# Optimization experiments

Measured on AMD Instinct MI355X. Metric: run time of the kernel, lower is better.

Reference implementation:

```python
import jax, jax.numpy as jnp
import numpy as np

B = 512      # graphs per batch
NPG = 62     # nodes (electrodes) per graph
N = B * NPG  # total nodes per band
F_IN = 5     # node features
H = 8        # attention heads
C = 3        # num_classes (GATConv out channels, concat=False)
DEG = 16     # avg degree
EG = NPG * DEG
E = B * EG   # edges per band
NB = 5       # bands: delta, alpha, beta, theta, gamma
DE_DIM = 930 # 310*3


def setup_inputs() -> dict:
    key = jax.random.key(0)
    ks = jax.random.split(key, 24)
    x_bands = jax.random.normal(ks[0], (NB, N, F_IN), dtype=jnp.float32)
    # within-graph random edges: node ids in [g*62, g*62+62)
    base = (jnp.arange(B, dtype=jnp.int32) * NPG)[None, :, None]
    src = jax.random.randint(ks[1], (NB, B, EG), 0, NPG, dtype=jnp.int32) + base
    dst = jax.random.randint(ks[2], (NB, B, EG), 0, NPG, dtype=jnp.int32) + base
    edge_index_bands = jnp.stack([src.reshape(NB, E), dst.reshape(NB, E)], axis=1)  # [NB,2,E]
    batch = jnp.repeat(jnp.arange(B, dtype=jnp.int32), NPG)  # [N]
    de = jax.random.normal(ks[3], (B, NPG, 5, 3), dtype=jnp.float32)
    s = 0.3
    params = dict(
        bn_gamma=jnp.ones((NB, F_IN), jnp.float32),
        bn_beta=jnp.zeros((NB, F_IN), jnp.float32),
        W=jax.random.normal(ks[4], (NB, F_IN, H * C)) * s,
        att_src=jax.random.normal(ks[5], (NB, H, C)) * s,
        att_dst=jax.random.normal(ks[6], (NB, H, C)) * s,
        gat_bias=jax.random.normal(ks[7], (NB, C)) * 0.01,
        fg_W=jax.random.normal(ks[8], (NB * C, 64)) * s,
        fg_b=jnp.zeros((64,), jnp.float32),
        ln_g=jnp.ones((DE_DIM,), jnp.float32),
        ln_b=jnp.zeros((DE_DIM,), jnp.float32),
        q_W=jax.random.normal(ks[9], (DE_DIM, 64)) * 0.03,
        q_b=jnp.zeros((64,), jnp.float32),
        k_W=jax.random.normal(ks[10], (DE_DIM, 64)) * 0.03,
        k_b=jnp.zeros((64,), jnp.float32),
        v_W=jax.random.normal(ks[11], (DE_DIM, 64)) * 0.03,
        v_b=jnp.zeros((64,), jnp.float32),
        fa_W=jax.random.normal(ks[12], (128, C)) * s,
        fa_b=jnp.zeros((C,), jnp.float32),
    )
    return dict(x_bands=x_bands, edge_index_bands=edge_index_bands, batch=batch, de=de, **params)


def _gat_band(x, ei, g, b, Wb, a_src, a_dst, bias, batch):
    # BatchNorm1d (training-mode batch stats), eps=1e-5
    mu = x.mean(0)
    var = x.var(0)
    xn = (x - mu) * jax.lax.rsqrt(var + 1e-5) * g + b
    # GATConv(F_IN -> C, heads=H, concat=False) with self-loops
    xt = (xn @ Wb).reshape(N, H, C)                       # [N,H,C]
    al_s = (xt * a_src).sum(-1)                           # [N,H]
    al_d = (xt * a_dst).sum(-1)                           # [N,H]
    loop = jnp.arange(N, dtype=ei.dtype)
    src = jnp.concatenate([ei[0], loop])                  # [E+N]
    dst = jnp.concatenate([ei[1], loop])
    e = jax.nn.leaky_relu(al_s[src] + al_d[dst], 0.2)     # [E+N,H]
    m = jax.ops.segment_max(e, dst, num_segments=N)
    ex = jnp.exp(e - m[dst])
    denom = jax.ops.segment_sum(ex, dst, num_segments=N)  # [N,H]
    msg = ex[:, :, None] * xt[src]                        # [E+N,H,C]
    out = jax.ops.segment_sum(msg, dst, num_segments=N) / denom[:, :, None]
    out = out.mean(1) + bias                              # concat=False -> head mean
    out = jax.nn.elu(out)
    # global_mean_pool
    summed = jax.ops.segment_sum(out, batch, num_segments=B)
    cnt = jax.ops.segment_sum(jnp.ones((N,), out.dtype), batch, num_segments=B)
    return summed / cnt[:, None]                          # [B,C]


def reference(x_bands, edge_index_bands, batch, de, bn_gamma, bn_beta, W,
              att_src, att_dst, gat_bias, fg_W, fg_b, ln_g, ln_b,
              q_W, q_b, k_W, k_b, v_W, v_b, fa_W, fa_b):
    pooled = jax.vmap(_gat_band, in_axes=(0, 0, 0, 0, 0, 0, 0, 0, None))(
        x_bands, edge_index_bands, bn_gamma, bn_beta, W, att_src, att_dst, gat_bias, batch
    )  # [NB,B,C]
    x_concat = jnp.transpose(pooled, (1, 0, 2)).reshape(B, NB * C)  # [B,15]
    x_out = jax.nn.elu(x_concat @ fg_W + fg_b)                       # [B,64]
    # de branch: LayerNorm + self-attention
    de_f = de.reshape(B, DE_DIM)
    mu = de_f.mean(-1, keepdims=True)
    var = de_f.var(-1, keepdims=True)
    de_n = (de_f - mu) * jax.lax.rsqrt(var + 1e-5) * ln_g + ln_b
    Q = de_n @ q_W + q_b
    K = de_n @ k_W + k_b
    V = de_n @ v_W + v_b
    attn = jax.nn.softmax(Q @ K.T / jnp.sqrt(jnp.float32(64)), axis=-1)
    x_de = attn @ V                                                  # [B,64]
    # F.leaky_relu(x, negative_slope=1) is the identity
    out = jnp.concatenate([x_out, x_de], axis=1) @ fa_W + fa_b       # [B,3]
    return jax.nn.elu(out)
```

## Files before the change

### kernel.cpp

```cpp
#include <hip/hip_runtime.h>
#include <math.h>

#define NBANDS 5
#define BATCH  512
#define NPG    62
#define NTOT   (BATCH*NPG)
#define F_IN   5
#define NH     8
#define NC     3
#define HC     (NH*NC)
#define EG     (NPG*16)
#define ETOT   (BATCH*EG)
#define EPG    (EG+NPG)
#define DE_DIM 930
#define KS     5
#define KLEN   186

#define GAT_BLOCKS  (BATCH*NBANDS)
#define QKVP_BLOCKS (128*3*KS)
#define MID_BLOCKS  (GAT_BLOCKS + QKVP_BLOCKS)

#define WS_BN     0
#define WS_LNS    512
#define WS_POOLED 1536
#define WS_Q      (WS_POOLED + NBANDS*BATCH*NC)
#define WS_KT     (WS_Q  + BATCH*64)
#define WS_V      (WS_KT + BATCH*64)
#define WS_PART   (WS_V  + BATCH*64)
#define WS_END    (WS_PART + 3*KS*BATCH*64)

__device__ __forceinline__ float eluf(float x) { return x > 0.f ? x : expm1f(x); }

__global__ __launch_bounds__(256) void stats_kernel(
    const float* __restrict__ x, const float* __restrict__ de,
    float* __restrict__ ws) {
    int bid = blockIdx.x;
    int tid = threadIdx.x;
    int w = tid >> 6, lane = tid & 63;
    if (bid < 40) {
        int band = bid >> 3, chunk = bid & 7;
        const int G4 = NTOT / 8 / 4;
        const float4* xb4 =
            (const float4*)(x + (size_t)band * NTOT * F_IN) + (size_t)chunk * G4 * 5;
        float s[F_IN] = {0,0,0,0,0}, q[F_IN] = {0,0,0,0,0};
        for (int gi = tid; gi < G4; gi += 256) {
            const float4* p4 = xb4 + (size_t)gi * 5;
            float vv[20];
            *(float4*)&vv[0]  = p4[0];
            *(float4*)&vv[4]  = p4[1];
            *(float4*)&vv[8]  = p4[2];
            *(float4*)&vv[12] = p4[3];
            *(float4*)&vv[16] = p4[4];
            #pragma unroll
            for (int i = 0; i < 20; ++i) { float v = vv[i]; s[i % 5] += v; q[i % 5] += v * v; }
        }
        #pragma unroll
        for (int f = 0; f < F_IN; ++f) {
            for (int off = 32; off; off >>= 1) {
                s[f] += __shfl_down(s[f], off, 64);
                q[f] += __shfl_down(q[f], off, 64);
            }
        }
        __shared__ float part[4][10];
        if (lane == 0) {
            #pragma unroll
            for (int f = 0; f < F_IN; ++f) { part[w][f] = s[f]; part[w][5 + f] = q[f]; }
        }
        __syncthreads();
        if (tid < 10) {
            float t = part[0][tid] + part[1][tid] + part[2][tid] + part[3][tid];
            ws[WS_BN + (band * 8 + chunk) * 10 + tid] = t;
        }
    } else {
        int r = (bid - 40) * 4 + w;
        const float* row = de + (size_t)r * DE_DIM;
        float s1 = 0.f, s2 = 0.f;
        for (int i = lane; i < DE_DIM; i += 64) { float v = row[i]; s1 += v; s2 += v * v; }
        #pragma unroll
        for (int off = 32; off; off >>= 1) {
            s1 += __shfl_down(s1, off, 64);
            s2 += __shfl_down(s2, off, 64);
        }
        if (lane == 0) {
            float mu  = s1 * (1.0f / DE_DIM);
            float var = s2 * (1.0f / DE_DIM) - mu * mu;
            ws[WS_LNS + r * 2]     = mu;
            ws[WS_LNS + r * 2 + 1] = rsqrtf(var + 1e-5f);
        }
    }
}

struct GatShared {
    float  Wl[F_IN * HC];
    float  attS[HC], attD[HC];
    float  bnsum[10];
    float  scale[F_IN], shift[F_IN];
    float  xns[NPG * F_IN];
    float4 xt4[NPG * NH];
    float  ald[NPG * NH];
    int    deg[NPG];
    int    offs[NPG + 1];
    int    cur[NPG];
    int    csr[EPG];
    float  outd[NPG][NC];
};
struct QkvShared { float dl[4][KLEN]; };

__global__ __launch_bounds__(256) void mid_kernel(
    const float* __restrict__ x, const int* __restrict__ ei,
    const float* __restrict__ bn_g, const float* __restrict__ bn_b,
    const float* __restrict__ Wg, const float* __restrict__ attSg,
    const float* __restrict__ attDg, const float* __restrict__ biasg,
    const float* __restrict__ de, const float* __restrict__ ln_g,
    const float* __restrict__ ln_b,
    const float* __restrict__ qW, const float* __restrict__ kW,
    const float* __restrict__ vW,
    const float* __restrict__ ws_in, float* __restrict__ ws_out) {
    __shared__ __align__(16) unsigned char smem[sizeof(GatShared)];
    int bid = blockIdx.x;
    int tid = threadIdx.x;

    if (bid < GAT_BLOCKS) {
        GatShared& S = *reinterpret_cast<GatShared*>(smem);
        int g    = bid & 511;
        int band = bid >> 9;
        int lane = tid & 63;
        int nbase = g * NPG;
        const float* wsbn = ws_in + WS_BN;
        float* pooled = ws_out + WS_POOLED;

        if (tid < F_IN * HC) S.Wl[tid] = Wg[band * F_IN * HC + tid];
        if (tid >= 128 && tid < 128 + HC) S.attS[tid - 128] = attSg[band * HC + tid - 128];
        if (tid >= 160 && tid < 160 + HC) S.attD[tid - 160] = attDg[band * HC + tid - 160];
        if (tid < NPG) S.deg[tid] = 0;
        if (tid >= 192 && tid < 202) {
            int f = tid - 192;
            float t = 0.f;
            #pragma unroll
            for (int c = 0; c < 8; ++c) t += wsbn[(band * 8 + c) * 10 + f];
            S.bnsum[f] = t;
        }
        __syncthreads();

        const int* srcp = ei + (size_t)band * 2 * ETOT + (size_t)g * EG;
        const int* dstp = srcp + ETOT;

        for (int e = tid; e < EG; e += 256) atomicAdd(&S.deg[dstp[e] - nbase], 1);
        if (tid < F_IN) {
            float mu  = S.bnsum[tid] * (1.0f / NTOT);
            float var = S.bnsum[5 + tid] * (1.0f / NTOT) - mu * mu;
            float sc  = rsqrtf(var + 1e-5f) * bn_g[band * F_IN + tid];
            S.scale[tid] = sc;
            S.shift[tid] = bn_b[band * F_IN + tid] - mu * sc;
        }
        __syncthreads();

        {
            const float* xr = x + (size_t)band * NTOT * F_IN + (size_t)nbase * F_IN;
            for (int i = tid; i < NPG * F_IN; i += 256) {
                int f = i % F_IN;
                S.xns[i] = xr[i] * S.scale[f] + S.shift[f];
            }
        }
        if (tid >= 64 && tid < 128) {
            int l = lane;
            int dv = (l < NPG) ? S.deg[l] + 1 : 0;
            int sc = dv;
            #pragma unroll
            for (int off = 1; off < 64; off <<= 1) {
                int t = __shfl_up(sc, off, 64);
                if (l >= off) sc += t;
            }
            if (l < NPG) S.offs[l + 1] = sc;
            if (l == 0)  S.offs[0] = 0;
        }
        __syncthreads();

        for (int p = tid; p < NPG * NH; p += 256) {
            int n = p >> 3, h = p & 7;
            float c0 = 0.f, c1 = 0.f, c2 = 0.f;
            #pragma unroll
            for (int f = 0; f < F_IN; ++f) {
                float xv = S.xns[n * F_IN + f];
                c0 += xv * S.Wl[f * HC + h * NC + 0];
                c1 += xv * S.Wl[f * HC + h * NC + 1];
                c2 += xv * S.Wl[f * HC + h * NC + 2];
            }
            float as = c0 * S.attS[h * NC] + c1 * S.attS[h * NC + 1] + c2 * S.attS[h * NC + 2];
            float ad = c0 * S.attD[h * NC] + c1 * S.attD[h * NC + 1] + c2 * S.attD[h * NC + 2];
            S.xt4[p] = make_float4(c0, c1, c2, as);
            S.ald[p] = ad;
        }
        if (tid < NPG) { int o0 = S.offs[tid]; S.csr[o0] = tid; S.cur[tid] = o0 + 1; }
        __syncthreads();

        for (int e = tid; e < EG; e += 256) {
            int ld = dstp[e] - nbase;
            int p = atomicAdd(&S.cur[ld], 1);
            S.csr[p] = srcp[e] - nbase;
        }
        __syncthreads();

        for (int p = tid; p < NPG * NH; p += 256) {
            int d = p >> 3, h = p & 7;
            int s0 = S.offs[d], s1 = S.offs[d + 1];
            float adv = S.ald[p];
            float den = 0.f, m0 = 0.f, m1 = 0.f, m2 = 0.f;
            for (int e = s0; e < s1; ++e) {
                int s = S.csr[e];
                float4 t = S.xt4[(s << 3) + h];
                float v = t.w + adv;
                v = v > 0.f ? v : 0.2f * v;
                float ex = __expf(v);
                den += ex;
                m0 += ex * t.x;
                m1 += ex * t.y;
                m2 += ex * t.z;
            }
            float rd = 1.0f / den;
            float o0 = m0 * rd, o1 = m1 * rd, o2 = m2 * rd;
            #pragma unroll
            for (int off = 1; off < 8; off <<= 1) {
                o0 += __shfl_xor(o0, off, 64);
                o1 += __shfl_xor(o1, off, 64);
                o2 += __shfl_xor(o2, off, 64);
            }
            if (h == 0) { S.outd[d][0] = o0; S.outd[d][1] = o1; S.outd[d][2] = o2; }
        }
        __syncthreads();

        float oc[NC] = {0.f, 0.f, 0.f};
        if (tid < NPG) {
            #pragma unroll
            for (int c = 0; c < NC; ++c)
                oc[c] = eluf(S.outd[tid][c] * (1.0f / NH) + biasg[band * NC + c]);
        }
        if (tid < 64) {
            #pragma unroll
            for (int c = 0; c < NC; ++c) {
                float v = oc[c];
                for (int off = 32; off; off >>= 1) v += __shfl_down(v, off, 64);
                if (tid == 0)
                    pooled[((size_t)band * BATCH + g) * NC + c] = v * (1.0f / NPG);
            }
        }
    } else {
        QkvShared& P = *reinterpret_cast<QkvShared*>(smem);
        int q  = bid - GAT_BLOCKS;
        int ks = q / 384;
        int r3 = q - ks * 384;
        int m  = r3 >> 7;
        int rt = r3 & 127;
        const float* lns = ws_in + WS_LNS;
        float* part = ws_out + WS_PART;

        int w = tid >> 6, col = tid & 63;
        for (int i = tid; i < 4 * KLEN; i += 256) {
            int rr = i / KLEN, ii = i - rr * KLEN;
            int row = rt * 4 + rr, gcol = ks * KLEN + ii;
            float mu = lns[row * 2], rstd = lns[row * 2 + 1];
            P.dl[rr][ii] = (de[(size_t)row * DE_DIM + gcol] - mu) * rstd * ln_g[gcol] + ln_b[gcol];
        }
        __syncthreads();
        const float* Wm = ((m == 0) ? qW : (m == 1) ? kW : vW) + (size_t)ks * KLEN * 64;
        float a[6] = {0, 0, 0, 0, 0, 0};
        for (int i = 0; i < KLEN; i += 6) {
            #pragma unroll
            for (int j = 0; j < 6; ++j)
                a[j] += P.dl[w][i + j] * Wm[(size_t)(i + j) * 64 + col];
        }
        float acc = ((a[0] + a[1]) + (a[2] + a[3])) + (a[4] + a[5]);
        part[(((size_t)m * KS + ks) * BATCH + rt * 4 + w) * 64 + col] = acc;
    }
}

__global__ __launch_bounds__(256) void qkv_reduce(
    const float* __restrict__ part,
    const float* __restrict__ qb, const float* __restrict__ kb,
    const float* __restrict__ vb,
    float* __restrict__ Q, float* __restrict__ KT, float* __restrict__ V) {
    int idx = blockIdx.x * 256 + threadIdx.x;
    int m  = idx >> 15;
    int local = idx & 32767;
    if (m == 1) {
        int row = local & 511, col = local >> 9;
        float s = 0.f;
        #pragma unroll
        for (int ks = 0; ks < KS; ++ks)
            s += part[(((size_t)KS + ks) << 15) + (row << 6) + col];
        KT[local] = s + kb[col];
    } else {
        int col = local & 63;
        float s = 0.f;
        #pragma unroll
        for (int ks = 0; ks < KS; ++ks)
            s += part[(((size_t)m * KS + ks) << 15) + local];
        s += (m == 0) ? qb[col] : vb[col];
        ((m == 0) ? Q : V)[local] = s;
    }
}

__global__ __launch_bounds__(256) void qkv_fused_fb(
    const float* __restrict__ de, const float* __restrict__ ln_g,
    const float* __restrict__ ln_b,
    const float* __restrict__ qW, const float* __restrict__ qb,
    const float* __restrict__ kW, const float* __restrict__ kb,
    const float* __restrict__ vW, const float* __restrict__ vb,
    float* __restrict__ Q, float* __restrict__ KT, float* __restrict__ V) {
    int r0 = blockIdx.x * 4;
    int m  = blockIdx.y;
    __shared__ float dn[4][DE_DIM];
    int tid  = threadIdx.x;
    int w    = tid >> 6, lane = tid & 63;
    const float* row = de + (size_t)(r0 + w) * DE_DIM;
    float s1 = 0.f, s2 = 0.f;
    for (int i = lane; i < DE_DIM; i += 64) {
        float v = row[i]; dn[w][i] = v; s1 += v; s2 += v * v;
    }
    #pragma unroll
    for (int off = 32; off; off >>= 1) {
        s1 += __shfl_down(s1, off, 64);
        s2 += __shfl_down(s2, off, 64);
    }
    float mu   = __shfl(s1, 0, 64) * (1.0f / DE_DIM);
    float var  = __shfl(s2, 0, 64) * (1.0f / DE_DIM) - mu * mu;
    float rstd = rsqrtf(var + 1e-5f);
    for (int i = lane; i < DE_DIM; i += 64)
        dn[w][i] = (dn[w][i] - mu) * rstd * ln_g[i] + ln_b[i];
    __syncthreads();
    const float* Wm = (m == 0) ? qW : (m == 1) ? kW : vW;
    const float* bm = (m == 0) ? qb : (m == 1) ? kb : vb;
    float a[10];
    #pragma unroll
    for (int j = 0; j < 10; ++j) a[j] = 0.f;
    for (int i = 0; i < DE_DIM; i += 10) {
        #pragma unroll
        for (int j = 0; j < 10; ++j)
            a[j] += dn[w][i + j] * Wm[(size_t)(i + j) * 64 + lane];
    }
    float acc = (((a[0] + a[1]) + (a[2] + a[3])) + ((a[4] + a[5]) + (a[6] + a[7])))
              + (a[8] + a[9]) + bm[lane];
    int r = r0 + w;
    if (m == 1) KT[lane * BATCH + r] = acc;
    else ((m == 0) ? Q : V)[(size_t)r * 64 + lane] = acc;
}

__global__ __launch_bounds__(256) void attn_final(
    const float* __restrict__ Q, const float* __restrict__ KT,
    const float* __restrict__ V, const float* __restrict__ pooled,
    const float* __restrict__ fgW, const float* __restrict__ fgb,
    const float* __restrict__ faW, const float* __restrict__ fab,
    float* __restrict__ out) {
    int b = blockIdx.x;
    int tid = threadIdx.x;
    __shared__ float qrow[64];
    __shared__ float p[BATCH];
    __shared__ float red[8];
    __shared__ float pv[4][64];
    __shared__ float xde[64], xout[64];
    if (tid < 64) qrow[tid] = Q[(size_t)b * 64 + tid];
    __syncthreads();

    float a0 = 0.f, a1 = 0.f, b0 = 0.f, b1 = 0.f;
    #pragma unroll 8
    for (int i = 0; i < 64; i += 2) {
        float q0 = qrow[i], q1 = qrow[i + 1];
        a0 += q0 * KT[(size_t)i * BATCH + tid];
        a1 += q1 * KT[(size_t)(i + 1) * BATCH + tid];
        b0 += q0 * KT[(size_t)i * BATCH + tid + 256];
        b1 += q1 * KT[(size_t)(i + 1) * BATCH + tid + 256];
    }
    float sj0 = (a0 + a1) * 0.125f, sj1 = (b0 + b1) * 0.125f;

    float mx = fmaxf(sj0, sj1);
    for (int off = 32; off; off >>= 1) mx = fmaxf(mx, __shfl_down(mx, off, 64));
    if ((tid & 63) == 0) red[tid >> 6] = mx;
    __syncthreads();
    mx = fmaxf(fmaxf(red[0], red[1]), fmaxf(red[2], red[3]));
    float e0 = __expf(sj0 - mx), e1 = __expf(sj1 - mx);
    p[tid] = e0; p[tid + 256] = e1;
    float s = e0 + e1;
    for (int off = 32; off; off >>= 1) s += __shfl_down(s, off, 64);
    if ((tid & 63) == 0) red[4 + (tid >> 6)] = s;
    __syncthreads();
    float denom = red[4] + red[5] + red[6] + red[7];

    int o = tid & 63, cq = tid >> 6;
    float acc = 0.f;
    #pragma unroll 4
    for (int j = cq * 128; j < cq * 128 + 128; ++j)
        acc += p[j] * V[(size_t)j * 64 + o];
    pv[cq][o] = acc;
    __syncthreads();
    if (tid < 64)
        xde[tid] = (pv[0][tid] + pv[1][tid] + pv[2][tid] + pv[3][tid]) / denom;
    if (tid >= 64 && tid < 128) {
        int oo = tid - 64;
        float a = fgb[oo];
        #pragma unroll
        for (int j = 0; j < NBANDS * NC; ++j) {
            int band = j / NC, c = j % NC;
            a += pooled[((size_t)band * BATCH + b) * NC + c] * fgW[j * 64 + oo];
        }
        xout[oo] = eluf(a);
    }
    __syncthreads();
    if (tid < NC) {
        float a = fab[tid];
        for (int i = 0; i < 64; ++i) a += xout[i] * faW[i * NC + tid];
        for (int i = 0; i < 64; ++i) a += xde[i] * faW[(64 + i) * NC + tid];
        out[(size_t)b * NC + tid] = eluf(a);
    }
}

extern "C" void kernel_launch(void* const* d_in, const int* in_sizes, int n_in,
                              void* d_out, int out_size, void* d_ws, size_t ws_size,
                              hipStream_t stream) {
    const float* x     = (const float*)d_in[0];
    const int*   ei    = (const int*)  d_in[1];
    const float* de    = (const float*)d_in[3];
    const float* bn_g  = (const float*)d_in[4];
    const float* bn_b  = (const float*)d_in[5];
    const float* W     = (const float*)d_in[6];
    const float* attS  = (const float*)d_in[7];
    const float* attD  = (const float*)d_in[8];
    const float* gbias = (const float*)d_in[9];
    const float* fgW   = (const float*)d_in[10];
    const float* fgb   = (const float*)d_in[11];
    const float* ln_g  = (const float*)d_in[12];
    const float* ln_b  = (const float*)d_in[13];
    const float* qW    = (const float*)d_in[14];
    const float* qb    = (const float*)d_in[15];
    const float* kW    = (const float*)d_in[16];
    const float* kb    = (const float*)d_in[17];
    const float* vW    = (const float*)d_in[18];
    const float* vb    = (const float*)d_in[19];
    const float* faW   = (const float*)d_in[20];
    const float* fab   = (const float*)d_in[21];
    float* ws  = (float*)d_ws;
    float* out = (float*)d_out;

    stats_kernel<<<168, 256, 0, stream>>>(x, de, ws);

    if (ws_size >= (size_t)WS_END * sizeof(float)) {
        mid_kernel<<<MID_BLOCKS, 256, 0, stream>>>(
            x, ei, bn_g, bn_b, W, attS, attD, gbias,
            de, ln_g, ln_b, qW, kW, vW, ws, ws);
        qkv_reduce<<<(3 * BATCH * 64) / 256, 256, 0, stream>>>(
            ws + WS_PART, qb, kb, vb, ws + WS_Q, ws + WS_KT, ws + WS_V);
    } else {
        mid_kernel<<<GAT_BLOCKS, 256, 0, stream>>>(
            x, ei, bn_g, bn_b, W, attS, attD, gbias,
            de, ln_g, ln_b, qW, kW, vW, ws, ws);
        qkv_fused_fb<<<dim3(BATCH / 4, 3), 256, 0, stream>>>(
            de, ln_g, ln_b, qW, qb, kW, kb, vW, vb,
            ws + WS_Q, ws + WS_KT, ws + WS_V);
    }
    attn_final<<<BATCH, 256, 0, stream>>>(ws + WS_Q, ws + WS_KT, ws + WS_V,
                                          ws + WS_POOLED, fgW, fgb, faW, fab, out);
}
```

Baseline: 78.16 us.

## Pad GAT feature table in LDS, shrink CSR to ushort, split block paths into noinline functions

Pads the per-node float4 feature table in shared memory to a stride of 9 heads, so the random neighbour gathers hit fewer LDS bank conflicts. Stores the CSR neighbour list as unsigned short to cut shared-memory footprint. Moves the GAT and QKV block paths into separate noinline device functions, so each path is register-allocated on its own. Also folds the BatchNorm scale computation into the first phase and reorders the barriers. That folding reads values written by other lanes of the same wave with no barrier in between, so it relies on in-order LDS execution within a wave.

```diff
diff --git a/kernel.cpp b/kernel.cpp
--- a/kernel.cpp
+++ b/kernel.cpp
@@ -15,6 +15,7 @@
 #define DE_DIM 930
 #define KS     5
 #define KLEN   186
+#define XTS    9
 
 #define GAT_BLOCKS  (BATCH*NBANDS)
 #define QKVP_BLOCKS (128*3*KS)
@@ -91,20 +92,185 @@
 }
 
 struct GatShared {
+    float4 xt4[NPG * XTS];
     float  Wl[F_IN * HC];
     float  attS[HC], attD[HC];
     float  bnsum[10];
     float  scale[F_IN], shift[F_IN];
     float  xns[NPG * F_IN];
-    float4 xt4[NPG * NH];
     float  ald[NPG * NH];
     int    deg[NPG];
     int    offs[NPG + 1];
     int    cur[NPG];
-    int    csr[EPG];
+    unsigned short csr[EPG];
     float  outd[NPG][NC];
 };
 struct QkvShared { float dl[4][KLEN]; };
+union  MidShared { GatShared g; QkvShared q; };
+
+__device__ __noinline__ void gat_path(
+    GatShared& S, int bid,
+    const float* __restrict__ x, const int* __restrict__ ei,
+    const float* __restrict__ bn_g, const float* __restrict__ bn_b,
+    const float* __restrict__ Wg, const float* __restrict__ attSg,
+    const float* __restrict__ attDg, const float* __restrict__ biasg,
+    const float* __restrict__ wsbn, float* __restrict__ pooled) {
+    int g    = bid & 511;
+    int band = bid >> 9;
+    int tid  = threadIdx.x;
+    int lane = tid & 63;
+    int nbase = g * NPG;
+
+    if (tid < F_IN * HC) S.Wl[tid] = Wg[band * F_IN * HC + tid];
+    if (tid >= 128 && tid < 128 + HC) S.attS[tid - 128] = attSg[band * HC + tid - 128];
+    if (tid >= 160 && tid < 160 + HC) S.attD[tid - 160] = attDg[band * HC + tid - 160];
+    if (tid < NPG) S.deg[tid] = 0;
+    if (tid >= 192 && tid < 202) {
+        int f = tid - 192;
+        float t = 0.f;
+        #pragma unroll
+        for (int c = 0; c < 8; ++c) t += wsbn[(band * 8 + c) * 10 + f];
+        S.bnsum[f] = t;
+    }
+    if (tid >= 192 && tid < 192 + F_IN) {
+        int f = tid - 192;
+        float mu  = S.bnsum[f] * (1.0f / NTOT);
+        float var = S.bnsum[5 + f] * (1.0f / NTOT) - mu * mu;
+        float sc  = rsqrtf(var + 1e-5f) * bn_g[band * F_IN + f];
+        S.scale[f] = sc;
+        S.shift[f] = bn_b[band * F_IN + f] - mu * sc;
+    }
+    __syncthreads();
+
+    const int* srcp = ei + (size_t)band * 2 * ETOT + (size_t)g * EG;
+    const int* dstp = srcp + ETOT;
+
+    for (int e = tid; e < EG; e += 256) atomicAdd(&S.deg[dstp[e] - nbase], 1);
+    {
+        const float* xr = x + (size_t)band * NTOT * F_IN + (size_t)nbase * F_IN;
+        for (int i = tid; i < NPG * F_IN; i += 256) {
+            int f = i % F_IN;
+            S.xns[i] = xr[i] * S.scale[f] + S.shift[f];
+        }
+    }
+    __syncthreads();
+
+    if (tid >= 64 && tid < 128) {
+        int l = lane;
+        int dv = (l < NPG) ? S.deg[l] + 1 : 0;
+        int sc = dv;
+        #pragma unroll
+        for (int off = 1; off < 64; off <<= 1) {
+            int t = __shfl_up(sc, off, 64);
+            if (l >= off) sc += t;
+        }
+        if (l < NPG) S.offs[l + 1] = sc;
+        if (l == 0)  S.offs[0] = 0;
+    }
+    for (int p = tid; p < NPG * NH; p += 256) {
+        int n = p >> 3, h = p & 7;
+        float c0 = 0.f, c1 = 0.f, c2 = 0.f;
+        #pragma unroll
+        for (int f = 0; f < F_IN; ++f) {
+            float xv = S.xns[n * F_IN + f];
+            c0 += xv * S.Wl[f * HC + h * NC + 0];
+            c1 += xv * S.Wl[f * HC + h * NC + 1];
+            c2 += xv * S.Wl[f * HC + h * NC + 2];
+        }
+        float as = c0 * S.attS[h * NC] + c1 * S.attS[h * NC + 1] + c2 * S.attS[h * NC + 2];
+        float ad = c0 * S.attD[h * NC] + c1 * S.attD[h * NC + 1] + c2 * S.attD[h * NC + 2];
+        S.xt4[n * XTS + h] = make_float4(c0, c1, c2, as);
+        S.ald[p] = ad;
+    }
+    __syncthreads();
+
+    if (tid < NPG) {
+        int o0 = S.offs[tid];
+        S.csr[o0] = (unsigned short)tid;
+        S.cur[tid] = o0 + 1;
+    }
+    __syncthreads();
+
+    for (int e = tid; e < EG; e += 256) {
+        int ld = dstp[e] - nbase;
+        int p = atomicAdd(&S.cur[ld], 1);
+        S.csr[p] = (unsigned short)(srcp[e] - nbase);
+    }
+    __syncthreads();
+
+    for (int p = tid; p < NPG * NH; p += 256) {
+        int d = p >> 3, h = p & 7;
+        int s0 = S.offs[d], s1 = S.offs[d + 1];
+        float adv = S.ald[p];
+        float den = 0.f, m0 = 0.f, m1 = 0.f, m2 = 0.f;
+        for (int e = s0; e < s1; ++e) {
+            int s = S.csr[e];
+            float4 t = S.xt4[s * XTS + h];
+            float v = t.w + adv;
+            v = fmaxf(v, 0.2f * v);
+            float ex = __expf(v);
+            den += ex;
+            m0 += ex * t.x;
+            m1 += ex * t.y;
+            m2 += ex * t.z;
+        }
+        float rd = 1.0f / den;
+        float o0 = m0 * rd, o1 = m1 * rd, o2 = m2 * rd;
+        #pragma unroll
+        for (int off = 1; off < 8; off <<= 1) {
+            o0 += __shfl_xor(o0, off, 64);
+            o1 += __shfl_xor(o1, off, 64);
+            o2 += __shfl_xor(o2, off, 64);
+        }
+        if (h == 0) { S.outd[d][0] = o0; S.outd[d][1] = o1; S.outd[d][2] = o2; }
+    }
+    __syncthreads();
+
+    float oc[NC] = {0.f, 0.f, 0.f};
+    if (tid < NPG) {
+        #pragma unroll
+        for (int c = 0; c < NC; ++c)
+            oc[c] = eluf(S.outd[tid][c] * (1.0f / NH) + biasg[band * NC + c]);
+    }
+    if (tid < 64) {
+        #pragma unroll
+        for (int c = 0; c < NC; ++c) {
+            float v = oc[c];
+            for (int off = 32; off; off >>= 1) v += __shfl_down(v, off, 64);
+            if (tid == 0)
+                pooled[((size_t)band * BATCH + g) * NC + c] = v * (1.0f / NPG);
+        }
+    }
+}
+
+__device__ __noinline__ void qkv_path(
+    QkvShared& P, int q,
+    const float* __restrict__ de, const float* __restrict__ lns,
+    const float* __restrict__ ln_g, const float* __restrict__ ln_b,
+    const float* __restrict__ qW, const float* __restrict__ kW,
+    const float* __restrict__ vW, float* __restrict__ part) {
+    int ks = q / 384;
+    int r3 = q - ks * 384;
+    int m  = r3 >> 7;
+    int rt = r3 & 127;
+    int tid = threadIdx.x, w = tid >> 6, col = tid & 63;
+    for (int i = tid; i < 4 * KLEN; i += 256) {
+        int rr = i / KLEN, ii = i - rr * KLEN;
+        int row = rt * 4 + rr, gcol = ks * KLEN + ii;
+        float mu = lns[row * 2], rstd = lns[row * 2 + 1];
+        P.dl[rr][ii] = (de[(size_t)row * DE_DIM + gcol] - mu) * rstd * ln_g[gcol] + ln_b[gcol];
+    }
+    __syncthreads();
+    const float* Wm = ((m == 0) ? qW : (m == 1) ? kW : vW) + (size_t)ks * KLEN * 64;
+    float a[6] = {0, 0, 0, 0, 0, 0};
+    for (int i = 0; i < KLEN; i += 6) {
+        #pragma unroll
+        for (int j = 0; j < 6; ++j)
+            a[j] += P.dl[w][i + j] * Wm[(size_t)(i + j) * 64 + col];
+    }
+    float acc = ((a[0] + a[1]) + (a[2] + a[3])) + (a[4] + a[5]);
+    part[(((size_t)m * KS + ks) * BATCH + rt * 4 + w) * 64 + col] = acc;
+}
 
 __global__ __launch_bounds__(256) void mid_kernel(
     const float* __restrict__ x, const int* __restrict__ ei,
@@ -116,161 +282,14 @@
     const float* __restrict__ qW, const float* __restrict__ kW,
     const float* __restrict__ vW,
     const float* __restrict__ ws_in, float* __restrict__ ws_out) {
-    __shared__ __align__(16) unsigned char smem[sizeof(GatShared)];
+    __shared__ MidShared S;
     int bid = blockIdx.x;
-    int tid = threadIdx.x;
-
     if (bid < GAT_BLOCKS) {
-        GatShared& S = *reinterpret_cast<GatShared*>(smem);
-        int g    = bid & 511;
-        int band = bid >> 9;
-        int lane = tid & 63;
-        int nbase = g * NPG;
-        const float* wsbn = ws_in + WS_BN;
-        float* pooled = ws_out + WS_POOLED;
-
-        if (tid < F_IN * HC) S.Wl[tid] = Wg[band * F_IN * HC + tid];
-        if (tid >= 128 && tid < 128 + HC) S.attS[tid - 128] = attSg[band * HC + tid - 128];
-        if (tid >= 160 && tid < 160 + HC) S.attD[tid - 160] = attDg[band * HC + tid - 160];
-        if (tid < NPG) S.deg[tid] = 0;
-        if (tid >= 192 && tid < 202) {
-            int f = tid - 192;
-            float t = 0.f;
-            #pragma unroll
-            for (int c = 0; c < 8; ++c) t += wsbn[(band * 8 + c) * 10 + f];
-            S.bnsum[f] = t;
-        }
-        __syncthreads();
-
-        const int* srcp = ei + (size_t)band * 2 * ETOT + (size_t)g * EG;
-        const int* dstp = srcp + ETOT;
-
-        for (int e = tid; e < EG; e += 256) atomicAdd(&S.deg[dstp[e] - nbase], 1);
-        if (tid < F_IN) {
-            float mu  = S.bnsum[tid] * (1.0f / NTOT);
-            float var = S.bnsum[5 + tid] * (1.0f / NTOT) - mu * mu;
-            float sc  = rsqrtf(var + 1e-5f) * bn_g[band * F_IN + tid];
-            S.scale[tid] = sc;
-            S.shift[tid] = bn_b[band * F_IN + tid] - mu * sc;
-        }
-        __syncthreads();
-
-        {
-            const float* xr = x + (size_t)band * NTOT * F_IN + (size_t)nbase * F_IN;
-            for (int i = tid; i < NPG * F_IN; i += 256) {
-                int f = i % F_IN;
-                S.xns[i] = xr[i] * S.scale[f] + S.shift[f];
-            }
-        }
-        if (tid >= 64 && tid < 128) {
-            int l = lane;
-            int dv = (l < NPG) ? S.deg[l] + 1 : 0;
-            int sc = dv;
-            #pragma unroll
-            for (int off = 1; off < 64; off <<= 1) {
-                int t = __shfl_up(sc, off, 64);
-                if (l >= off) sc += t;
-            }
-            if (l < NPG) S.offs[l + 1] = sc;
-            if (l == 0)  S.offs[0] = 0;
-        }
-        __syncthreads();
-
-        for (int p = tid; p < NPG * NH; p += 256) {
-            int n = p >> 3, h = p & 7;
-            float c0 = 0.f, c1 = 0.f, c2 = 0.f;
-            #pragma unroll
-            for (int f = 0; f < F_IN; ++f) {
-                float xv = S.xns[n * F_IN + f];
-                c0 += xv * S.Wl[f * HC + h * NC + 0];
-                c1 += xv * S.Wl[f * HC + h * NC + 1];
-                c2 += xv * S.Wl[f * HC + h * NC + 2];
-            }
-            float as = c0 * S.attS[h * NC] + c1 * S.attS[h * NC + 1] + c2 * S.attS[h * NC + 2];
-            float ad = c0 * S.attD[h * NC] + c1 * S.attD[h * NC + 1] + c2 * S.attD[h * NC + 2];
-            S.xt4[p] = make_float4(c0, c1, c2, as);
-            S.ald[p] = ad;
-        }
-        if (tid < NPG) { int o0 = S.offs[tid]; S.csr[o0] = tid; S.cur[tid] = o0 + 1; }
-        __syncthreads();
-
-        for (int e = tid; e < EG; e += 256) {
-            int ld = dstp[e] - nbase;
-            int p = atomicAdd(&S.cur[ld], 1);
-            S.csr[p] = srcp[e] - nbase;
-        }
-        __syncthreads();
-
-        for (int p = tid; p < NPG * NH; p += 256) {
-            int d = p >> 3, h = p & 7;
-            int s0 = S.offs[d], s1 = S.offs[d + 1];
-            float adv = S.ald[p];
-            float den = 0.f, m0 = 0.f, m1 = 0.f, m2 = 0.f;
-            for (int e = s0; e < s1; ++e) {
-                int s = S.csr[e];
-                float4 t = S.xt4[(s << 3) + h];
-                float v = t.w + adv;
-                v = v > 0.f ? v : 0.2f * v;
-                float ex = __expf(v);
-                den += ex;
-                m0 += ex * t.x;
-                m1 += ex * t.y;
-                m2 += ex * t.z;
-            }
-            float rd = 1.0f / den;
-            float o0 = m0 * rd, o1 = m1 * rd, o2 = m2 * rd;
-            #pragma unroll
-            for (int off = 1; off < 8; off <<= 1) {
-                o0 += __shfl_xor(o0, off, 64);
-                o1 += __shfl_xor(o1, off, 64);
-                o2 += __shfl_xor(o2, off, 64);
-            }
-            if (h == 0) { S.outd[d][0] = o0; S.outd[d][1] = o1; S.outd[d][2] = o2; }
-        }
-        __syncthreads();
-
-        float oc[NC] = {0.f, 0.f, 0.f};
-        if (tid < NPG) {
-            #pragma unroll
-            for (int c = 0; c < NC; ++c)
-                oc[c] = eluf(S.outd[tid][c] * (1.0f / NH) + biasg[band * NC + c]);
-        }
-        if (tid < 64) {
-            #pragma unroll
-            for (int c = 0; c < NC; ++c) {
-                float v = oc[c];
-                for (int off = 32; off; off >>= 1) v += __shfl_down(v, off, 64);
-                if (tid == 0)
-                    pooled[((size_t)band * BATCH + g) * NC + c] = v * (1.0f / NPG);
-            }
-        }
+        gat_path(S.g, bid, x, ei, bn_g, bn_b, Wg, attSg, attDg, biasg,
+                 ws_in + WS_BN, ws_out + WS_POOLED);
     } else {
-        QkvShared& P = *reinterpret_cast<QkvShared*>(smem);
-        int q  = bid - GAT_BLOCKS;
-        int ks = q / 384;
-        int r3 = q - ks * 384;
-        int m  = r3 >> 7;
-        int rt = r3 & 127;
-        const float* lns = ws_in + WS_LNS;
-        float* part = ws_out + WS_PART;
-
-        int w = tid >> 6, col = tid & 63;
-        for (int i = tid; i < 4 * KLEN; i += 256) {
-            int rr = i / KLEN, ii = i - rr * KLEN;
-            int row = rt * 4 + rr, gcol = ks * KLEN + ii;
-            float mu = lns[row * 2], rstd = lns[row * 2 + 1];
-            P.dl[rr][ii] = (de[(size_t)row * DE_DIM + gcol] - mu) * rstd * ln_g[gcol] + ln_b[gcol];
-        }
-        __syncthreads();
-        const float* Wm = ((m == 0) ? qW : (m == 1) ? kW : vW) + (size_t)ks * KLEN * 64;
-        float a[6] = {0, 0, 0, 0, 0, 0};
-        for (int i = 0; i < KLEN; i += 6) {
-            #pragma unroll
-            for (int j = 0; j < 6; ++j)
-                a[j] += P.dl[w][i + j] * Wm[(size_t)(i + j) * 64 + col];
-        }
-        float acc = ((a[0] + a[1]) + (a[2] + a[3])) + (a[4] + a[5]);
-        part[(((size_t)m * KS + ks) * BATCH + rt * 4 + w) * 64 + col] = acc;
+        qkv_path(S.q, bid - GAT_BLOCKS, de, ws_in + WS_LNS, ln_g, ln_b,
+                 qW, kW, vW, ws_out + WS_PART);
     }
 }
 
```

New measurement: 103.4 us. 32.2% more time.
